# Kernel optimization log

Measured on AMD Instinct MI355X. Metric: run time of the kernel, lower is better.

The kernel has to match this reference:

```python
import jax, jax.numpy as jnp
import numpy as np

B, S, D = 2, 2048, 2048
H, KVH, HD = 16, 4, 128
REP = H // KVH  # 4
THETA = 10000.0


def setup_inputs() -> dict:
    key = jax.random.key(0)
    ks = jax.random.split(key, 5)
    scale = 0.02
    x = jax.random.normal(ks[0], (B, S, D), dtype=jnp.float32)
    Wq = jax.random.normal(ks[1], (D, H * HD), dtype=jnp.float32) * scale
    Wk = jax.random.normal(ks[2], (D, KVH * HD), dtype=jnp.float32) * scale
    Wv = jax.random.normal(ks[3], (D, KVH * HD), dtype=jnp.float32) * scale
    Wo = jax.random.normal(ks[4], (H * HD, D), dtype=jnp.float32) * scale
    return {"x": x, "Wq": Wq, "Wk": Wk, "Wv": Wv, "Wo": Wo}


def _rope_cos_sin(seq_len, dtype):
    # HF-style rotary embedding: inv_freq over even dims, duplicated halves
    inv_freq = 1.0 / (THETA ** (jnp.arange(0, HD, 2, dtype=jnp.float32) / HD))
    pos = jnp.arange(seq_len, dtype=jnp.float32)
    ang = pos[:, None] * inv_freq[None, :]          # [S, HD/2]
    emb = jnp.concatenate([ang, ang], axis=-1)       # [S, HD]
    return jnp.cos(emb).astype(dtype), jnp.sin(emb).astype(dtype)


def _rotate_half(t):
    t1, t2 = jnp.split(t, 2, axis=-1)
    return jnp.concatenate([-t2, t1], axis=-1)


def reference(x, Wq, Wk, Wv, Wo):
    bsz, seq_len, _ = x.shape
    q = (x @ Wq).reshape(bsz, seq_len, H, HD).transpose(0, 2, 1, 3)    # [B,H,S,HD]
    k = (x @ Wk).reshape(bsz, seq_len, KVH, HD).transpose(0, 2, 1, 3)  # [B,KVH,S,HD]
    v = (x @ Wv).reshape(bsz, seq_len, KVH, HD).transpose(0, 2, 1, 3)
    cos, sin = _rope_cos_sin(seq_len, q.dtype)       # [S,HD]
    cos = cos[None, None, :, :]
    sin = sin[None, None, :, :]
    q = q * cos + _rotate_half(q) * sin
    k = k * cos + _rotate_half(k) * sin
    # repeat_interleave KV heads to match Q heads
    k = jnp.repeat(k, REP, axis=1)                   # [B,H,S,HD]
    v = jnp.repeat(v, REP, axis=1)
    scores = jnp.einsum('bhqd,bhkd->bhqk', q, k) / jnp.sqrt(jnp.float32(HD)).astype(q.dtype)
    i = jnp.arange(seq_len)
    causal = jnp.where(i[None, :] > i[:, None], jnp.float32(-jnp.inf), 0.0).astype(scores.dtype)
    scores = scores + causal[None, None, :, :]
    probs = jax.nn.softmax(scores.astype(jnp.float32), axis=-1).astype(q.dtype)
    out = jnp.einsum('bhqk,bhkd->bhqd', probs, v)    # [B,H,S,HD]
    out = out.transpose(0, 2, 1, 3).reshape(bsz, seq_len, H * HD)
    return out @ Wo
```

## Files before the change

kernel.cpp:

```cpp
#include <hip/hip_runtime.h>
#include <math.h>

#define B_   2
#define S_   2048
#define D_   2048
#define H_   16
#define KVH_ 4
#define HD_  128
#define REP_ 4

typedef __attribute__((ext_vector_type(8))) short bf16x8;
typedef __attribute__((ext_vector_type(4))) short bf16x4;
typedef __attribute__((ext_vector_type(4))) float f32x4;

#define QSCALE_LOG2E 0.1275266977097153f

__device__ __forceinline__ unsigned short f2bf(float x) {
    union { float f; unsigned u; } v; v.f = x;
    unsigned r = v.u + 0x7FFF + ((v.u >> 16) & 1);
    return (unsigned short)(r >> 16);
}

__device__ __forceinline__ unsigned short f2bf_fast(float x) {
    union { float f; unsigned u; } v; v.f = x;
    return (unsigned short)((v.u + 0x8000) >> 16);
}

__device__ __forceinline__ void gl_lds16(const unsigned short* g, unsigned short* l) {
    __builtin_amdgcn_global_load_lds(
        (const __attribute__((address_space(1))) unsigned int*)g,
        (__attribute__((address_space(3))) unsigned int*)l,
        16, 0, 0);
}

#define PH_BAR() do { asm volatile("" ::: "memory"); \
                      __builtin_amdgcn_s_barrier();  \
                      asm volatile("" ::: "memory"); } while (0)
#define VMW6 asm volatile("s_waitcnt vmcnt(6)" ::: "memory")
#define VMW4 asm volatile("s_waitcnt vmcnt(4)" ::: "memory")
#define VMW0 asm volatile("s_waitcnt vmcnt(0)" ::: "memory")

__global__ void cast_bf16(const float* __restrict__ src,
                          unsigned short* __restrict__ dst, int n4)
{
    int i = blockIdx.x * 256 + threadIdx.x;
    if (i >= n4) return;
    float4 v = *(const float4*)&src[(size_t)i * 4];
    bf16x4 o;
    o[0] = (short)f2bf(v.x); o[1] = (short)f2bf(v.y);
    o[2] = (short)f2bf(v.z); o[3] = (short)f2bf(v.w);
    *(bf16x4*)&dst[(size_t)i * 4] = o;
}

__global__ __launch_bounds__(256) void cast_transpose_all(
    const float* __restrict__ Wq, const float* __restrict__ Wk,
    const float* __restrict__ Wv, const float* __restrict__ Wo,
    unsigned short* __restrict__ Wqt, unsigned short* __restrict__ Wkt,
    unsigned short* __restrict__ Wvt, unsigned short* __restrict__ Wot)
{
    __shared__ float T[32][33];
    const int y = blockIdx.y;
    const float* src; unsigned short* dst; int C, bj;
    if (y < 64)      { src = Wq; dst = Wqt; C = 2048; bj = y; }
    else if (y < 80) { src = Wk; dst = Wkt; C = 512;  bj = y - 64; }
    else if (y < 96) { src = Wv; dst = Wvt; C = 512;  bj = y - 80; }
    else             { src = Wo; dst = Wot; C = 2048; bj = y - 96; }

    const int bi = blockIdx.x;
    const int t  = threadIdx.x;
    const int r  = t >> 3, cq = (t & 7) * 4;

    float4 v = *(const float4*)&src[(size_t)(bi * 32 + r) * C + bj * 32 + cq];
    T[r][cq + 0] = v.x; T[r][cq + 1] = v.y;
    T[r][cq + 2] = v.z; T[r][cq + 3] = v.w;
    __syncthreads();

    bf16x4 o;
    o[0] = (short)f2bf(T[cq + 0][r]);
    o[1] = (short)f2bf(T[cq + 1][r]);
    o[2] = (short)f2bf(T[cq + 2][r]);
    o[3] = (short)f2bf(T[cq + 3][r]);
    *(bf16x4*)&dst[(size_t)(bj * 32 + r) * 2048 + bi * 32 + cq] = o;
}

__global__ __launch_bounds__(512, 2) void qkv_mfma8(
    const unsigned short* __restrict__ Ah,
    const unsigned short* __restrict__ Wqt,
    const unsigned short* __restrict__ Wkt,
    const unsigned short* __restrict__ Wvt,
    unsigned short* __restrict__ Qh, unsigned short* __restrict__ Kh,
    unsigned short* __restrict__ Vt)
{
    __shared__ __align__(16) unsigned short lds[65536];

    const int bid = blockIdx.x;
    const int swz = (bid & 7) * 24 + (bid >> 3);
    const int bm = swz / 12, bn = swz % 12;
    const int m0 = bm * 256, n0 = bn * 256;

    const int tid  = threadIdx.x;
    const int w    = tid >> 6;
    const int lane = tid & 63;
    const int lo16 = lane & 15, quad = lane >> 4;
    const int wm   = w >> 2, wn = w & 3;

    const unsigned short* Bt;
    if (n0 < 2048)      Bt = Wqt + (size_t)n0 * 2048;
    else if (n0 < 2560) Bt = Wkt + (size_t)(n0 - 2048) * 2048;
    else                Bt = Wvt + (size_t)(n0 - 2560) * 2048;
    const unsigned short* Ag   = Ah + (size_t)m0 * 2048;
    const unsigned short* AgH1 = Ag + (size_t)128 * 2048;
    const unsigned short* BtH1 = Bt + (size_t)128 * 2048;

    const int rs   = lane >> 3;
    const int sce  = (((lane & 7) ^ rs) << 3);
    const int grow = w * 8 + rs;

    #define STAGE(gb, k0, lb) do {                                          \
        const unsigned short* _g = (gb) + (size_t)grow * 2048 + (k0) + sce; \
        gl_lds16(_g,                     (lb) + w * 512);                   \
        gl_lds16(_g + (size_t)64 * 2048, (lb) + (8 + w) * 512);             \
    } while (0)

    const int swb = (lo16 & 7) << 4;
    const int ac0 = (quad << 4) ^ swb;
    const int ac1 = (64 | (quad << 4)) ^ swb;
    char* ldsb = (char*)lds;
    const int abase = (wm * 128 + lo16) * 128;
    const int bbase = (wn * 16 + lo16) * 128 + 32768;

    f32x4 acc[8][4];
    #pragma unroll
    for (int mf = 0; mf < 8; ++mf)
        #pragma unroll
        for (int j = 0; j < 4; ++j) acc[mf][j] = (f32x4){0.f, 0.f, 0.f, 0.f};

    bf16x8 a0[4][2], a1[4][2], b0[2][2], b1[2][2];

    #define MM(Aa, Bb, mo, jo)                                               \
        _Pragma("unroll") for (int mf = 0; mf < 4; ++mf)                     \
        _Pragma("unroll") for (int j = 0; j < 2; ++j) {                      \
            acc[(mo)+mf][(jo)+j] = __builtin_amdgcn_mfma_f32_16x16x32_bf16(  \
                Aa[mf][0], Bb[j][0], acc[(mo)+mf][(jo)+j], 0, 0, 0);         \
            acc[(mo)+mf][(jo)+j] = __builtin_amdgcn_mfma_f32_16x16x32_bf16(  \
                Aa[mf][1], Bb[j][1], acc[(mo)+mf][(jo)+j], 0, 0, 0);         \
        }

    STAGE(Bt,   0,  lds + 16384);
    STAGE(BtH1, 0,  lds + 24576);
    STAGE(Ag,   0,  lds + 0);
    STAGE(AgH1, 0,  lds + 8192);
    STAGE(Bt,   64, lds + 32768 + 16384);
    STAGE(BtH1, 64, lds + 32768 + 24576);
    STAGE(Ag,   64, lds + 32768);
    VMW6;
    PH_BAR();

    #define PHASES(p, t)                                                         \
    {   _Pragma("unroll") for (int mf = 0; mf < 4; ++mf) {                       \
            a0[mf][0] = *(const bf16x8*)(ldsb + (p)*65536 + abase + mf*2048 + ac0); \
            a0[mf][1] = *(const bf16x8*)(ldsb + (p)*65536 + abase + mf*2048 + ac1); \
        }                                                                        \
        _Pragma("unroll") for (int j = 0; j < 2; ++j) {                          \
            b0[j][0] = *(const bf16x8*)(ldsb + (p)*65536 + bbase + j*8192 + ac0); \
            b0[j][1] = *(const bf16x8*)(ldsb + (p)*65536 + bbase + j*8192 + ac1); \
        }                                                                        \
        STAGE(AgH1, ((t)+1)*64, lds + ((p)^1)*32768 + 8192);                     \
        PH_BAR(); __builtin_amdgcn_s_setprio(1);                                 \
        MM(a0, b0, 0, 0);                                                        \
        __builtin_amdgcn_s_setprio(0); PH_BAR();                                 \
        _Pragma("unroll") for (int j = 0; j < 2; ++j) {                          \
            b1[j][0] = *(const bf16x8*)(ldsb + (p)*65536 + bbase + (j+2)*8192 + ac0); \
            b1[j][1] = *(const bf16x8*)(ldsb + (p)*65536 + bbase + (j+2)*8192 + ac1); \
        }                                                                        \
        STAGE(Bt, ((t)+2)*64, lds + (p)*32768 + 16384);                          \
        PH_BAR(); __builtin_amdgcn_s_setprio(1);                                 \
        MM(a0, b1, 0, 2);                                                        \
        __builtin_amdgcn_s_setprio(0); PH_BAR();                                 \
        _Pragma("unroll") for (int mf = 0; mf < 4; ++mf) {                       \
            a1[mf][0] = *(const bf16x8*)(ldsb + (p)*65536 + abase + (mf+4)*2048 + ac0); \
            a1[mf][1] = *(const bf16x8*)(ldsb + (p)*65536 + abase + (mf+4)*2048 + ac1); \
        }                                                                        \
        STAGE(BtH1, ((t)+2)*64, lds + (p)*32768 + 24576);                        \
        PH_BAR(); __builtin_amdgcn_s_setprio(1);                                 \
        MM(a1, b0, 4, 0);                                                        \
        __builtin_amdgcn_s_setprio(0); PH_BAR();                                 \
        STAGE(Ag, ((t)+2)*64, lds + (p)*32768);                                  \
        PH_BAR(); __builtin_amdgcn_s_setprio(1);                                 \
        MM(a1, b1, 4, 2);                                                        \
        __builtin_amdgcn_s_setprio(0);                                           \
        VMW6;                                                                    \
        PH_BAR();                                                                \
    }

    for (int it = 0; it < 16; ++it) {
        const int t = 2 * it;
        PHASES(0, t);
        PHASES(1, t + 1);
    }

    VMW0;
    PH_BAR();

    const int bb = m0 >> 11;
    const int s0loc = m0 & 2047;

    if (n0 < 2560) {
        const bool isQ = (n0 < 2048);
        const int h0 = isQ ? (n0 >> 7) : ((n0 - 2048) >> 7);
        const float post = isQ ? QSCALE_LOG2E : 1.0f;
        unsigned short* db[2];
        #pragma unroll
        for (int hp = 0; hp < 2; ++hp)
            db[hp] = isQ
                ? Qh + (((size_t)bb * H_   + h0 + hp) * S_) * HD_
                : Kh + (((size_t)bb * KVH_ + h0 + hp) * S_) * HD_;
        const int d = wn * 16 + lo16;
        const float inv = exp2f(-(float)d * 0.20761871093344086f);
        #pragma unroll
        for (int mf = 0; mf < 8; ++mf) {
            #pragma unroll
            for (int r = 0; r < 4; ++r) {
                int s = s0loc + wm * 128 + mf * 16 + quad * 4 + r;
                float sn, c;
                sincosf((float)s * inv, &sn, &c);
                #pragma unroll
                for (int hp = 0; hp < 2; ++hp) {
                    float lo = acc[mf][2 * hp + 0][r];
                    float hi = acc[mf][2 * hp + 1][r];
                    unsigned short* drow = db[hp] + (size_t)s * HD_;
                    drow[d]      = f2bf((lo * c - hi * sn) * post);
                    drow[d + 64] = f2bf((hi * c + lo * sn) * post);
                }
            }
        }
    } else {
        const int g0 = (n0 - 2560) >> 7;
        unsigned short* Ts = lds;
        const int d = wn * 16 + lo16;
        #pragma unroll
        for (int hp = 0; hp < 2; ++hp) {
            if (hp) PH_BAR();
            #pragma unroll
            for (int mf = 0; mf < 8; ++mf) {
                int ml = wm * 128 + mf * 16 + quad * 4;
                bf16x4 v0, v1;
                #pragma unroll
                for (int r = 0; r < 4; ++r) {
                    v0[r] = (short)f2bf(acc[mf][2 * hp + 0][r]);
                    v1[r] = (short)f2bf(acc[mf][2 * hp + 1][r]);
                }
                *(bf16x4*)&Ts[(size_t)d        * 264 + ml] = v0;
                *(bf16x4*)&Ts[(size_t)(d + 64) * 264 + ml] = v1;
            }
            PH_BAR();
            unsigned short* dstb = Vt + (((size_t)bb * KVH_ + g0 + hp) * HD_) * S_ + s0loc;
            #pragma unroll
            for (int itb = 0; itb < 8; ++itb) {
                int dd = itb * 16 + (tid >> 5);
                int ch = (tid & 31) * 8;
                *(bf16x8*)(dstb + (size_t)dd * S_ + ch) =
                    *(const bf16x8*)&Ts[(size_t)dd * 264 + ch];
            }
        }
    }
    #undef PHASES
    #undef MM
    #undef STAGE
}

__global__ __launch_bounds__(256, 2) void flash_attn_mfma(
    const unsigned short* __restrict__ Qh,
    const unsigned short* __restrict__ Kh,
    const unsigned short* __restrict__ Vt,
    unsigned short* __restrict__ attb)
{
    const int bh   = blockIdx.x;
    const int yy   = blockIdx.y;
    const int qt   = (yy < 8) ? (15 - yy) : (yy - 8);
    const int b    = bh >> 4, h = bh & 15;
    const int g    = h >> 2;
    const int tid  = threadIdx.x;
    const int w    = tid >> 6;
    const int lane = tid & 63;
    const int lo16 = lane & 15;
    const int quad = lane >> 4;

    const unsigned short* Qb = Qh + (((size_t)b * H_   + h) * S_) * HD_;
    const unsigned short* Kb = Kh + (((size_t)b * KVH_ + g) * S_) * HD_;
    const unsigned short* Vb = Vt + (((size_t)b * KVH_ + g) * HD_) * S_;

    __shared__ __align__(16) unsigned short Ks[64][136];
    __shared__ __align__(16) unsigned short Vs[128][72];
    __shared__ __align__(16) unsigned short Ps[4][32][72];

    const int q0 = qt * 128;
    const int qw = q0 + w * 32;

    bf16x8 qf[2][4];
    #pragma unroll
    for (int st = 0; st < 2; ++st)
        #pragma unroll
        for (int kc = 0; kc < 4; ++kc)
            qf[st][kc] = *(const bf16x8*)(Qb + (size_t)(qw + st * 16 + lo16) * HD_
                                             + kc * 32 + quad * 8);

    f32x4 o[2][8];
    #pragma unroll
    for (int st = 0; st < 2; ++st)
        #pragma unroll
        for (int n = 0; n < 8; ++n) o[st][n] = (f32x4){0.f, 0.f, 0.f, 0.f};
    float l_loc[2][4];
    #pragma unroll
    for (int st = 0; st < 2; ++st)
        #pragma unroll
        for (int r = 0; r < 4; ++r) l_loc[st][r] = 0.0f;

    const int kr = tid >> 4, kch = (tid & 15) * 8;
    const int vr = tid >> 3, vch = (tid & 7) * 8;

    bf16x8 kreg[4], vreg[4];
    #pragma unroll
    for (int i = 0; i < 4; ++i) {
        kreg[i] = *(const bf16x8*)(Kb + (size_t)(16 * i + kr) * HD_ + kch);
        vreg[i] = *(const bf16x8*)(Vb + (size_t)(32 * i + vr) * S_ + vch);
    }

    const int ktend = 2 * qt + 1;
    for (int kt = 0; kt <= ktend; ++kt) {
        const int k0 = kt * 64;
        asm volatile("s_barrier" ::: "memory");
        #pragma unroll
        for (int i = 0; i < 4; ++i) {
            *(bf16x8*)&Ks[16 * i + kr][kch] = kreg[i];
            *(bf16x8*)&Vs[32 * i + vr][vch] = vreg[i];
        }
        if (kt < ktend) {
            const int k0n = k0 + 64;
            #pragma unroll
            for (int i = 0; i < 4; ++i) {
                kreg[i] = *(const bf16x8*)(Kb + (size_t)(k0n + 16 * i + kr) * HD_ + kch);
                vreg[i] = *(const bf16x8*)(Vb + (size_t)(32 * i + vr) * S_ + k0n + vch);
            }
        }
        asm volatile("s_waitcnt lgkmcnt(0)" ::: "memory");
        asm volatile("s_barrier" ::: "memory");

        if (w >= 2 || kt < ktend) {
            f32x4 sc[2][4];
            #pragma unroll
            for (int st = 0; st < 2; ++st)
                #pragma unroll
                for (int cb = 0; cb < 4; ++cb) sc[st][cb] = (f32x4){0.f, 0.f, 0.f, 0.f};
            #pragma unroll
            for (int kc = 0; kc < 4; ++kc)
                #pragma unroll
                for (int cb = 0; cb < 4; ++cb) {
                    bf16x8 kf = *(const bf16x8*)&Ks[cb * 16 + lo16][kc * 32 + quad * 8];
                    #pragma unroll
                    for (int st = 0; st < 2; ++st)
                        sc[st][cb] = __builtin_amdgcn_mfma_f32_16x16x32_bf16(
                            qf[st][kc], kf, sc[st][cb], 0, 0, 0);
                }

            const bool masked = (w < 2) ? (kt == 2 * qt) : (kt == ktend);
            if (masked) {
                #pragma unroll
                for (int st = 0; st < 2; ++st)
                    #pragma unroll
                    for (int r = 0; r < 4; ++r) {
                        const int row = qw + st * 16 + quad * 4 + r;
                        float lacc = 0.0f;
                        #pragma unroll
                        for (int cb = 0; cb < 4; ++cb) {
                            float xv = sc[st][cb][r];
                            if ((k0 + cb * 16 + lo16) > row) xv = -1e30f;
                            float p = exp2f(xv);
                            lacc += p;
                            Ps[w][st * 16 + quad * 4 + r][cb * 16 + lo16] = f2bf_fast(p);
                        }
                        l_loc[st][r] += lacc;
                    }
            } else {
                #pragma unroll
                for (int st = 0; st < 2; ++st)
                    #pragma unroll
                    for (int r = 0; r < 4; ++r) {
                        float lacc = 0.0f;
                        #pragma unroll
                        for (int cb = 0; cb < 4; ++cb) {
                            float p = exp2f(sc[st][cb][r]);
                            lacc += p;
                            Ps[w][st * 16 + quad * 4 + r][cb * 16 + lo16] = f2bf_fast(p);
                        }
                        l_loc[st][r] += lacc;
                    }
            }

            #pragma unroll
            for (int kc = 0; kc < 2; ++kc) {
                bf16x8 pf[2];
                #pragma unroll
                for (int st = 0; st < 2; ++st)
                    pf[st] = *(const bf16x8*)&Ps[w][st * 16 + lo16][kc * 32 + quad * 8];
                #pragma unroll
                for (int n = 0; n < 8; ++n) {
                    bf16x8 vf = *(const bf16x8*)&Vs[n * 16 + lo16][kc * 32 + quad * 8];
                    #pragma unroll
                    for (int st = 0; st < 2; ++st)
                        o[st][n] = __builtin_amdgcn_mfma_f32_16x16x32_bf16(
                            pf[st], vf, o[st][n], 0, 0, 0);
                }
            }
        }
    }

    #pragma unroll
    for (int st = 0; st < 2; ++st)
        #pragma unroll
        for (int r = 0; r < 4; ++r) {
            float l = l_loc[st][r];
            l += __shfl_xor(l, 1);
            l += __shfl_xor(l, 2);
            l += __shfl_xor(l, 4);
            l += __shfl_xor(l, 8);
            float invl = 1.0f / l;
            int srow = qw + st * 16 + quad * 4 + r;
            unsigned short* dst = attb + ((size_t)b * S_ + srow) * D_ + h * HD_;
            #pragma unroll
            for (int n = 0; n < 8; ++n)
                dst[n * 16 + lo16] = f2bf(o[st][n][r] * invl);
        }
}

__global__ __launch_bounds__(512, 2) void out_mfma8(
    const unsigned short* __restrict__ Ah,
    const unsigned short* __restrict__ Wot,
    float* __restrict__ C)
{
    __shared__ __align__(16) unsigned short lds[49152];

    const int bid = blockIdx.x;
    const int swz = (bid & 7) * 32 + (bid >> 3);
    const int bm = swz >> 4, bn = swz & 15;
    const int m0 = bm * 256, n0 = bn * 128;

    const int tid  = threadIdx.x;
    const int w    = tid >> 6;
    const int lane = tid & 63;
    const int lo16 = lane & 15, quad = lane >> 4;
    const int wm   = w >> 2, wn = w & 3;

    const unsigned short* Ag   = Ah  + (size_t)m0 * 2048;
    const unsigned short* AgH1 = Ag  + (size_t)128 * 2048;
    const unsigned short* Bt   = Wot + (size_t)n0 * 2048;

    const int rs   = lane >> 3;
    const int sce  = (((lane & 7) ^ rs) << 3);
    const int grow = w * 8 + rs;

    #define OSTAGE(gb, k0, lb) do {                                         \
        const unsigned short* _g = (gb) + (size_t)grow * 2048 + (k0) + sce; \
        gl_lds16(_g,                     (lb) + w * 512);                   \
        gl_lds16(_g + (size_t)64 * 2048, (lb) + (8 + w) * 512);             \
    } while (0)

    const int swb = (lo16 & 7) << 4;
    const int ac0 = (quad << 4) ^ swb;
    const int ac1 = (64 | (quad << 4)) ^ swb;
    char* ldsb = (char*)lds;
    const int abase = (wm * 128 + lo16) * 128;
    const int bbase = (wn * 32 + lo16) * 128 + 32768;

    f32x4 acc[8][2];
    #pragma unroll
    for (int mf = 0; mf < 8; ++mf)
        #pragma unroll
        for (int j = 0; j < 2; ++j) acc[mf][j] = (f32x4){0.f, 0.f, 0.f, 0.f};

    bf16x8 a0[4][2], a1[4][2], bb[2][2];

    #define OMM(Aa, mo, j)                                                   \
        _Pragma("unroll") for (int mf = 0; mf < 4; ++mf) {                   \
            acc[(mo)+mf][j] = __builtin_amdgcn_mfma_f32_16x16x32_bf16(       \
                Aa[mf][0], bb[j][0], acc[(mo)+mf][j], 0, 0, 0);              \
            acc[(mo)+mf][j] = __builtin_amdgcn_mfma_f32_16x16x32_bf16(       \
                Aa[mf][1], bb[j][1], acc[(mo)+mf][j], 0, 0, 0);              \
        }

    OSTAGE(Bt,   0,  lds + 16384);
    OSTAGE(Ag,   0,  lds + 0);
    OSTAGE(AgH1, 0,  lds + 8192);
    OSTAGE(Bt,   64, lds + 24576 + 16384);
    OSTAGE(Ag,   64, lds + 24576);
    VMW4;
    PH_BAR();

    #define OPH(p, t)                                                            \
    {   _Pragma("unroll") for (int mf = 0; mf < 4; ++mf) {                       \
            a0[mf][0] = *(const bf16x8*)(ldsb + (p)*49152 + abase + mf*2048 + ac0); \
            a0[mf][1] = *(const bf16x8*)(ldsb + (p)*49152 + abase + mf*2048 + ac1); \
        }                                                                        \
        _Pragma("unroll") for (int j = 0; j < 2; ++j) {                          \
            bb[j][0] = *(const bf16x8*)(ldsb + (p)*49152 + bbase + j*2048 + ac0); \
            bb[j][1] = *(const bf16x8*)(ldsb + (p)*49152 + bbase + j*2048 + ac1); \
        }                                                                        \
        OSTAGE(AgH1, ((t)+1)*64, lds + ((p)^1)*24576 + 8192);                    \
        PH_BAR(); __builtin_amdgcn_s_setprio(1);                                 \
        OMM(a0, 0, 0);                                                           \
        __builtin_amdgcn_s_setprio(0); PH_BAR();                                 \
        OSTAGE(Bt, ((t)+2)*64, lds + (p)*24576 + 16384);                         \
        PH_BAR(); __builtin_amdgcn_s_setprio(1);                                 \
        OMM(a0, 0, 1);                                                           \
        __builtin_amdgcn_s_setprio(0); PH_BAR();                                 \
        _Pragma("unroll") for (int mf = 0; mf < 4; ++mf) {                       \
            a1[mf][0] = *(const bf16x8*)(ldsb + (p)*49152 + abase + (mf+4)*2048 + ac0); \
            a1[mf][1] = *(const bf16x8*)(ldsb + (p)*49152 + abase + (mf+4)*2048 + ac1); \
        }                                                                        \
        PH_BAR(); __builtin_amdgcn_s_setprio(1);                                 \
        OMM(a1, 4, 0);                                                           \
        __builtin_amdgcn_s_setprio(0); PH_BAR();                                 \
        OSTAGE(Ag, ((t)+2)*64, lds + (p)*24576);                                 \
        PH_BAR(); __builtin_amdgcn_s_setprio(1);                                 \
        OMM(a1, 4, 1);                                                           \
        __builtin_amdgcn_s_setprio(0);                                           \
        VMW4;                                                                    \
        PH_BAR();                                                                \
    }

    for (int it = 0; it < 16; ++it) {
        const int t = 2 * it;
        OPH(0, t);
        OPH(1, t + 1);
    }

    VMW0;

    #pragma unroll
    for (int mf = 0; mf < 8; ++mf)
        #pragma unroll
        for (int r = 0; r < 4; ++r) {
            size_t m = (size_t)(m0 + wm * 128 + mf * 16 + quad * 4 + r);
            #pragma unroll
            for (int j = 0; j < 2; ++j)
                C[m * 2048 + n0 + wn * 32 + j * 16 + lo16] = acc[mf][j][r];
        }
    #undef OPH
    #undef OMM
    #undef OSTAGE
}

extern "C" void kernel_launch(void* const* d_in, const int* in_sizes, int n_in,
                              void* d_out, int out_size, void* d_ws, size_t ws_size,
                              hipStream_t stream)
{
    const float* x  = (const float*)d_in[0];
    const float* Wq = (const float*)d_in[1];
    const float* Wk = (const float*)d_in[2];
    const float* Wv = (const float*)d_in[3];
    const float* Wo = (const float*)d_in[4];
    float* out = (float*)d_out;

    unsigned short* xh  = (unsigned short*)d_ws;
    unsigned short* Wqt = xh  + (size_t)4096 * 2048;
    unsigned short* Wkt = Wqt + (size_t)2048 * 2048;
    unsigned short* Wvt = Wkt + (size_t)512 * 2048;
    unsigned short* Wot = Wvt + (size_t)512 * 2048;
    unsigned short* Qh  = Wot + (size_t)2048 * 2048;
    unsigned short* Kh  = Qh  + (size_t)B_ * H_   * S_ * HD_;
    unsigned short* Vt  = Kh  + (size_t)B_ * KVH_ * S_ * HD_;
    unsigned short* attb= xh;

    cast_bf16<<<(4096 * 2048 / 4 + 255) / 256, 256, 0, stream>>>(x, xh, 4096 * 2048 / 4);
    cast_transpose_all<<<dim3(64, 160), 256, 0, stream>>>(Wq, Wk, Wv, Wo, Wqt, Wkt, Wvt, Wot);

    qkv_mfma8<<<192, 512, 0, stream>>>(xh, Wqt, Wkt, Wvt, Qh, Kh, Vt);

    flash_attn_mfma<<<dim3(32, 16), 256, 0, stream>>>(Qh, Kh, Vt, attb);

    out_mfma8<<<256, 512, 0, stream>>>(attb, Wot, out);
}
```

Baseline: 278.7 us.

## Split flash attention across eight waves and XOR-swizzle K/V shared tiles

Result: slower. 293.2 us (+5.2%).

```diff
diff --git a/kernel.cpp b/kernel.cpp
--- a/kernel.cpp
+++ b/kernel.cpp
@@ -269,7 +269,7 @@
     #undef STAGE
 }
 
-__global__ __launch_bounds__(256, 2) void flash_attn_mfma(
+__global__ __launch_bounds__(512, 4) void flash_attn_mfma(
     const unsigned short* __restrict__ Qh,
     const unsigned short* __restrict__ Kh,
     const unsigned short* __restrict__ Vt,
@@ -292,38 +292,34 @@
 
     __shared__ __align__(16) unsigned short Ks[64][136];
     __shared__ __align__(16) unsigned short Vs[128][72];
-    __shared__ __align__(16) unsigned short Ps[4][32][72];
+    __shared__ __align__(16) unsigned short Ps[8][16][72];
 
     const int q0 = qt * 128;
-    const int qw = q0 + w * 32;
-
-    bf16x8 qf[2][4];
-    #pragma unroll
-    for (int st = 0; st < 2; ++st)
-        #pragma unroll
-        for (int kc = 0; kc < 4; ++kc)
-            qf[st][kc] = *(const bf16x8*)(Qb + (size_t)(qw + st * 16 + lo16) * HD_
-                                             + kc * 32 + quad * 8);
-
-    f32x4 o[2][8];
-    #pragma unroll
-    for (int st = 0; st < 2; ++st)
-        #pragma unroll
-        for (int n = 0; n < 8; ++n) o[st][n] = (f32x4){0.f, 0.f, 0.f, 0.f};
-    float l_loc[2][4];
-    #pragma unroll
-    for (int st = 0; st < 2; ++st)
-        #pragma unroll
-        for (int r = 0; r < 4; ++r) l_loc[st][r] = 0.0f;
-
-    const int kr = tid >> 4, kch = (tid & 15) * 8;
-    const int vr = tid >> 3, vch = (tid & 7) * 8;
-
-    bf16x8 kreg[4], vreg[4];
-    #pragma unroll
-    for (int i = 0; i < 4; ++i) {
-        kreg[i] = *(const bf16x8*)(Kb + (size_t)(16 * i + kr) * HD_ + kch);
-        vreg[i] = *(const bf16x8*)(Vb + (size_t)(32 * i + vr) * S_ + vch);
+    const int qw = q0 + w * 16;
+
+    bf16x8 qf[4];
+    #pragma unroll
+    for (int kc = 0; kc < 4; ++kc)
+        qf[kc] = *(const bf16x8*)(Qb + (size_t)(qw + lo16) * HD_ + kc * 32 + quad * 8);
+
+    f32x4 o[8];
+    #pragma unroll
+    for (int n = 0; n < 8; ++n) o[n] = (f32x4){0.f, 0.f, 0.f, 0.f};
+    float l_loc[4];
+    #pragma unroll
+    for (int r = 0; r < 4; ++r) l_loc[r] = 0.0f;
+
+    const int kr  = tid >> 4, kcu = tid & 15;
+    const int vr  = tid >> 3, vcu = tid & 7;
+    const int ksw = ((kcu ^ (kr & 7)) * 8);
+    const int vsw = ((vcu ^ (vr & 7)) * 8);
+    const int rsw = (lo16 & 7);
+
+    bf16x8 kreg[2], vreg[2];
+    #pragma unroll
+    for (int i = 0; i < 2; ++i) {
+        kreg[i] = *(const bf16x8*)(Kb + (size_t)(32 * i + kr) * HD_ + kcu * 8);
+        vreg[i] = *(const bf16x8*)(Vb + (size_t)(64 * i + vr) * S_ + vcu * 8);
     }
 
     const int ktend = 2 * qt + 1;
@@ -331,106 +327,93 @@
         const int k0 = kt * 64;
         asm volatile("s_barrier" ::: "memory");
         #pragma unroll
-        for (int i = 0; i < 4; ++i) {
-            *(bf16x8*)&Ks[16 * i + kr][kch] = kreg[i];
-            *(bf16x8*)&Vs[32 * i + vr][vch] = vreg[i];
+        for (int i = 0; i < 2; ++i) {
+            *(bf16x8*)&Ks[32 * i + kr][ksw] = kreg[i];
+            *(bf16x8*)&Vs[64 * i + vr][vsw] = vreg[i];
         }
         if (kt < ktend) {
             const int k0n = k0 + 64;
             #pragma unroll
-            for (int i = 0; i < 4; ++i) {
-                kreg[i] = *(const bf16x8*)(Kb + (size_t)(k0n + 16 * i + kr) * HD_ + kch);
-                vreg[i] = *(const bf16x8*)(Vb + (size_t)(32 * i + vr) * S_ + k0n + vch);
+            for (int i = 0; i < 2; ++i) {
+                kreg[i] = *(const bf16x8*)(Kb + (size_t)(k0n + 32 * i + kr) * HD_ + kcu * 8);
+                vreg[i] = *(const bf16x8*)(Vb + (size_t)(64 * i + vr) * S_ + k0n + vcu * 8);
             }
         }
         asm volatile("s_waitcnt lgkmcnt(0)" ::: "memory");
         asm volatile("s_barrier" ::: "memory");
 
-        if (w >= 2 || kt < ktend) {
-            f32x4 sc[2][4];
-            #pragma unroll
-            for (int st = 0; st < 2; ++st)
-                #pragma unroll
-                for (int cb = 0; cb < 4; ++cb) sc[st][cb] = (f32x4){0.f, 0.f, 0.f, 0.f};
+        if (w >= 4 || kt < ktend) {
+            f32x4 sc[4];
+            #pragma unroll
+            for (int cb = 0; cb < 4; ++cb) sc[cb] = (f32x4){0.f, 0.f, 0.f, 0.f};
             #pragma unroll
             for (int kc = 0; kc < 4; ++kc)
                 #pragma unroll
                 for (int cb = 0; cb < 4; ++cb) {
-                    bf16x8 kf = *(const bf16x8*)&Ks[cb * 16 + lo16][kc * 32 + quad * 8];
-                    #pragma unroll
-                    for (int st = 0; st < 2; ++st)
-                        sc[st][cb] = __builtin_amdgcn_mfma_f32_16x16x32_bf16(
-                            qf[st][kc], kf, sc[st][cb], 0, 0, 0);
+                    bf16x8 kf = *(const bf16x8*)&Ks[cb * 16 + lo16]
+                                                   [((kc * 4 + quad) ^ rsw) * 8];
+                    sc[cb] = __builtin_amdgcn_mfma_f32_16x16x32_bf16(
+                        qf[kc], kf, sc[cb], 0, 0, 0);
                 }
 
-            const bool masked = (w < 2) ? (kt == 2 * qt) : (kt == ktend);
+            const bool masked = (w < 4) ? (kt == 2 * qt) : (kt == ktend);
             if (masked) {
                 #pragma unroll
-                for (int st = 0; st < 2; ++st)
+                for (int r = 0; r < 4; ++r) {
+                    const int row = qw + quad * 4 + r;
+                    float lacc = 0.0f;
                     #pragma unroll
-                    for (int r = 0; r < 4; ++r) {
-                        const int row = qw + st * 16 + quad * 4 + r;
-                        float lacc = 0.0f;
-                        #pragma unroll
-                        for (int cb = 0; cb < 4; ++cb) {
-                            float xv = sc[st][cb][r];
-                            if ((k0 + cb * 16 + lo16) > row) xv = -1e30f;
-                            float p = exp2f(xv);
-                            lacc += p;
-                            Ps[w][st * 16 + quad * 4 + r][cb * 16 + lo16] = f2bf_fast(p);
-                        }
-                        l_loc[st][r] += lacc;
+                    for (int cb = 0; cb < 4; ++cb) {
+                        float xv = sc[cb][r];
+                        if ((k0 + cb * 16 + lo16) > row) xv = -1e30f;
+                        float p = exp2f(xv);
+                        lacc += p;
+                        Ps[w][quad * 4 + r][cb * 16 + lo16] = f2bf_fast(p);
                     }
+                    l_loc[r] += lacc;
+                }
             } else {
                 #pragma unroll
-                for (int st = 0; st < 2; ++st)
+                for (int r = 0; r < 4; ++r) {
+                    float lacc = 0.0f;
                     #pragma unroll
-                    for (int r = 0; r < 4; ++r) {
-                        float lacc = 0.0f;
-                        #pragma unroll
-                        for (int cb = 0; cb < 4; ++cb) {
-                            float p = exp2f(sc[st][cb][r]);
-                            lacc += p;
-                            Ps[w][st * 16 + quad * 4 + r][cb * 16 + lo16] = f2bf_fast(p);
-                        }
-                        l_loc[st][r] += lacc;
+                    for (int cb = 0; cb < 4; ++cb) {
+                        float p = exp2f(sc[cb][r]);
+                        lacc += p;
+                        Ps[w][quad * 4 + r][cb * 16 + lo16] = f2bf_fast(p);
                     }
+                    l_loc[r] += lacc;
+                }
             }
 
             #pragma unroll
             for (int kc = 0; kc < 2; ++kc) {
-                bf16x8 pf[2];
-                #pragma unroll
-                for (int st = 0; st < 2; ++st)
-                    pf[st] = *(const bf16x8*)&Ps[w][st * 16 + lo16][kc * 32 + quad * 8];
+                bf16x8 pf = *(const bf16x8*)&Ps[w][lo16][kc * 32 + quad * 8];
                 #pragma unroll
                 for (int n = 0; n < 8; ++n) {
-                    bf16x8 vf = *(const bf16x8*)&Vs[n * 16 + lo16][kc * 32 + quad * 8];
-                    #pragma unroll
-                    for (int st = 0; st < 2; ++st)
-                        o[st][n] = __builtin_amdgcn_mfma_f32_16x16x32_bf16(
-                            pf[st], vf, o[st][n], 0, 0, 0);
+                    bf16x8 vf = *(const bf16x8*)&Vs[n * 16 + lo16]
+                                                   [((kc * 4 + quad) ^ rsw) * 8];
+                    o[n] = __builtin_amdgcn_mfma_f32_16x16x32_bf16(
+                        pf, vf, o[n], 0, 0, 0);
                 }
             }
         }
     }
 
     #pragma unroll
-    for (int st = 0; st < 2; ++st)
-        #pragma unroll
-        for (int r = 0; r < 4; ++r) {
-            float l = l_loc[st][r];
-            l += __shfl_xor(l, 1);
-            l += __shfl_xor(l, 2);
-            l += __shfl_xor(l, 4);
-            l += __shfl_xor(l, 8);
-            float invl = 1.0f / l;
-            int srow = qw + st * 16 + quad * 4 + r;
-            unsigned short* dst = attb + ((size_t)b * S_ + srow) * D_ + h * HD_;
-            #pragma unroll
-            for (int n = 0; n < 8; ++n)
-                dst[n * 16 + lo16] = f2bf(o[st][n][r] * invl);
-        }
+    for (int r = 0; r < 4; ++r) {
+        float l = l_loc[r];
+        l += __shfl_xor(l, 1);
+        l += __shfl_xor(l, 2);
+        l += __shfl_xor(l, 4);
+        l += __shfl_xor(l, 8);
+        float invl = 1.0f / l;
+        int srow = qw + quad * 4 + r;
+        unsigned short* dst = attb + ((size_t)b * S_ + srow) * D_ + h * HD_;
+        #pragma unroll
+        for (int n = 0; n < 8; ++n)
+            dst[n * 16 + lo16] = f2bf(o[n][r] * invl);
+    }
 }
 
 __global__ __launch_bounds__(512, 2) void out_mfma8(
@@ -576,7 +559,7 @@
 
     qkv_mfma8<<<192, 512, 0, stream>>>(xh, Wqt, Wkt, Wvt, Qh, Kh, Vt);
 
-    flash_attn_mfma<<<dim3(32, 16), 256, 0, stream>>>(Qh, Kh, Vt, attb);
+    flash_attn_mfma<<<dim3(32, 16), 512, 0, stream>>>(Qh, Kh, Vt, attb);
 
     out_mfma8<<<256, 512, 0, stream>>>(attb, Wot, out);
 }
```
